# Kernel tuning notes

Measured on AMD Instinct MI355X. Metric: run time of the kernel, lower is better.

## Reference

```python
import jax, jax.numpy as jnp
import numpy as np

B, T, C, H = 512, 256, 512, 64  # batch, block_size, n_embedding, head_size


def setup_inputs() -> dict:
    key = jax.random.key(0)
    kx, kq, kk, kv = jax.random.split(key, 4)
    # nn.Linear(C, H, bias=False) default init ~ U(-1/sqrt(C), 1/sqrt(C)); stored as x @ W
    s = 1.0 / np.sqrt(C)
    return {
        "x": jax.random.normal(kx, (B, T, C), dtype=jnp.float32),
        "Wq": jax.random.uniform(kq, (C, H), jnp.float32, -s, s),
        "Wk": jax.random.uniform(kk, (C, H), jnp.float32, -s, s),
        "Wv": jax.random.uniform(kv, (C, H), jnp.float32, -s, s),
    }


def reference(x, Wq, Wk, Wv):
    # Projections (bias=False Linear)
    q = x @ Wq  # [B,T,H]
    k = x @ Wk  # [B,T,H]
    v = x @ Wv  # [B,T,H]
    scale = k.shape[-1] ** -0.5
    wei = jnp.einsum('bqh,bkh->bqk', q, k) * scale  # [B,T,T]
    causal = jnp.tril(jnp.ones((x.shape[1], x.shape[1]), dtype=bool))
    wei = jnp.where(causal, wei, -jnp.inf)
    wei = jax.nn.softmax(wei, axis=-1)
    # dropout p=0.0 (eval-mode reference) -> identity
    return wei @ v  # [B,T,H]
```

## Files before the change

kernel.cpp:

```cpp
#include <hip/hip_runtime.h>
#include <hip/hip_bf16.h>

typedef __bf16 bf16;
typedef __bf16 bf16x8 __attribute__((ext_vector_type(8)));
typedef __bf16 bf16x4 __attribute__((ext_vector_type(4)));
typedef float  f32x4  __attribute__((ext_vector_type(4)));

#define MFMA16(a,b,c) __builtin_amdgcn_mfma_f32_16x16x32_bf16((a),(b),(c),0,0,0)

__device__ __forceinline__ void gld16(const void* g, void* l) {
    __builtin_amdgcn_global_load_lds(
        (const __attribute__((address_space(1))) void*)g,
        (__attribute__((address_space(3))) void*)l, 16, 0, 0);
}


__global__ void __launch_bounds__(256) wt_frag_kernel(
        const float* __restrict__ Wq, const float* __restrict__ Wk,
        const float* __restrict__ Wv, bf16* __restrict__ WTfrag) {
    int tid = blockIdx.x * 256 + threadIdx.x;
    int j  = tid & 7;
    int l  = (tid >> 3) & 63;
    int f  = tid >> 9;
    int nf = f % 12;
    int KC = f / 12;
    int k   = KC * 32 + (l >> 4) * 8 + j;
    int col = (nf & 3) * 16 + (l & 15);
    const float* W = (nf < 4) ? Wq : ((nf < 8) ? Wk : Wv);
    WTfrag[tid] = (bf16)W[k * 64 + col];
}

__global__ void __launch_bounds__(256, 2) fused_kernel(
        const float* __restrict__ x, const bf16* __restrict__ WTfrag,
        float* __restrict__ out) {
    extern __shared__ char smem[];

    const int tid = threadIdx.x;
    const int l   = tid & 63;
    const int w   = tid >> 6;
    const int lo  = l & 15;
    const int hi  = l >> 4;
    const int b   = blockIdx.x;
    const char* xb = (const char*)x + (size_t)b * 524288;
    const char* wb = (const char*)WTfrag;

    f32x4 acc[4][12];
    #pragma unroll
    for (int mq = 0; mq < 4; ++mq)
        #pragma unroll
        for (int nf = 0; nf < 12; ++nf)
            acc[mq][nf] = (f32x4){0.f, 0.f, 0.f, 0.f};

    #pragma unroll 1
    for (int kc = 0; kc < 16; ++kc) {
        #pragma unroll
        for (int j = 0; j < 8; ++j) {
            const int s   = j * 256 + tid;
            const int row = s >> 3;
            const int uP  = s & 7;
            const int uL  = uP ^ (row & 7);
            gld16(xb + (size_t)row * 2048 + kc * 128 + uL * 16,
                  smem + s * 16);
        }
        #pragma unroll
        for (int j = 0; j < 3; ++j) {
            const int s = j * 256 + tid;
            gld16(wb + kc * 12288 + s * 16, smem + 32768 + s * 16);
        }
        __syncthreads();

        bf16x8 a[4];
        #pragma unroll
        for (int mq = 0; mq < 4; ++mq) {
            const int row = mq * 64 + w * 16 + lo;
            const int u0  = (hi * 2)     ^ (lo & 7);
            const int u1  = (hi * 2 + 1) ^ (lo & 7);
            f32x4 v0 = *(const f32x4*)(smem + row * 128 + u0 * 16);
            f32x4 v1 = *(const f32x4*)(smem + row * 128 + u1 * 16);
            bf16x8 t;
            t[0] = (bf16)v0[0]; t[1] = (bf16)v0[1]; t[2] = (bf16)v0[2]; t[3] = (bf16)v0[3];
            t[4] = (bf16)v1[0]; t[5] = (bf16)v1[1]; t[6] = (bf16)v1[2]; t[7] = (bf16)v1[3];
            a[mq] = t;
        }
        #pragma unroll
        for (int nf = 0; nf < 12; ++nf) {
            bf16x8 bf_ = *(const bf16x8*)(smem + 32768 + nf * 1024 + l * 16);
            #pragma unroll
            for (int mq = 0; mq < 4; ++mq)
                acc[mq][nf] = MFMA16(a[mq], bf_, acc[mq][nf]);
        }
        __syncthreads();
    }

    char* Kb = smem;
    char* Vb = smem + 32768;
    #pragma unroll
    for (int nf = 4; nf < 12; ++nf) {
        #pragma unroll
        for (int mq = 0; mq < 4; ++mq) {
            if (nf < 8) {
                #pragma unroll
                for (int i = 0; i < 4; ++i) {
                    bf16 v = (bf16)acc[mq][nf][i];
                    const int row = mq * 64 + w * 16 + hi * 4 + i;
                    const int col = (nf - 4) * 16 + lo;
                    const int u   = col >> 3;
                    *(bf16*)(Kb + row * 128 + ((u ^ (row & 7)) << 4) +
                             (col & 7) * 2) = v;
                }
            } else {
                const int h  = (nf - 8) * 16 + lo;
                const int tb = mq * 64 + w * 16 + hi * 4;
                const int u  = tb >> 3;
                bf16x4 pk;
                pk[0] = (bf16)acc[mq][nf][0]; pk[1] = (bf16)acc[mq][nf][1];
                pk[2] = (bf16)acc[mq][nf][2]; pk[3] = (bf16)acc[mq][nf][3];
                *(bf16x4*)(Vb + h * 512 + ((u ^ (h & 7)) << 4) +
                           (tb & 7) * 2) = pk;
            }
        }
    }

    bf16* Pl = (bf16*)(smem + 65536) + w * 1152;
    bf16x8 qfr[4][2];
    #pragma unroll
    for (int qf = 0; qf < 4; ++qf) {
        #pragma unroll
        for (int nf = 0; nf < 4; ++nf)
            #pragma unroll
            for (int i = 0; i < 4; ++i)
                Pl[(hi * 4 + i) * 72 + nf * 16 + lo] = (bf16)acc[qf][nf][i];
        #pragma unroll
        for (int ks = 0; ks < 2; ++ks)
            qfr[qf][ks] = *(const bf16x8*)(Pl + lo * 72 + ks * 32 + hi * 8);
    }
    __syncthreads();

    f32x4 o[4][4];
    #pragma unroll
    for (int qf = 0; qf < 4; ++qf)
        #pragma unroll
        for (int mf = 0; mf < 4; ++mf)
            o[qf][mf] = (f32x4){0.f, 0.f, 0.f, 0.f};
    float m2[4]   = {-INFINITY, -INFINITY, -INFINITY, -INFINITY};
    float lsum[4] = {0.f, 0.f, 0.f, 0.f};

    const float SC = 0.125f * 1.44269504088896340736f;

    #pragma unroll
    for (int kc = 0; kc < 4; ++kc) {
        bf16x8 vf[4][2];
        #pragma unroll
        for (int mf = 0; mf < 4; ++mf)
            #pragma unroll
            for (int ks = 0; ks < 2; ++ks) {
                const int h = mf * 16 + lo;
                const int u = kc * 8 + ks * 4 + hi;
                vf[mf][ks] = *(const bf16x8*)(Vb + h * 512 + ((u ^ (lo & 7)) << 4));
            }

        #pragma unroll
        for (int qf = kc; qf < 4; ++qf) {
            f32x4 s[4];
            #pragma unroll
            for (int kf = 0; kf < 4; ++kf) {
                const int key = kc * 64 + kf * 16 + lo;
                bf16x8 k0 = *(const bf16x8*)(Kb + key * 128 + ((hi ^ (lo & 7)) << 4));
                bf16x8 k1 = *(const bf16x8*)(Kb + key * 128 + (((4 + hi) ^ (lo & 7)) << 4));
                f32x4 t = (f32x4){0.f, 0.f, 0.f, 0.f};
                t = MFMA16(k0, qfr[qf][0], t);
                t = MFMA16(k1, qfr[qf][1], t);
                s[kf] = t;
            }
            float mx = -INFINITY;
            #pragma unroll
            for (int kf = 0; kf < 4; ++kf)
                #pragma unroll
                for (int i = 0; i < 4; ++i) {
                    float v = s[kf][i] * SC;
                    if (kc == qf && (kf * 16 + hi * 4 + i) > (w * 16 + lo)) v = -INFINITY;
                    s[kf][i] = v;
                    mx = fmaxf(mx, v);
                }
            mx = fmaxf(mx, __shfl_xor(mx, 16));
            mx = fmaxf(mx, __shfl_xor(mx, 32));
            const float mnew = fmaxf(m2[qf], mx);
            const float rsc  = exp2f(m2[qf] - mnew);
            m2[qf] = mnew;

            float cs = 0.f;
            bf16x4 pk[4];
            #pragma unroll
            for (int kf = 0; kf < 4; ++kf)
                #pragma unroll
                for (int i = 0; i < 4; ++i) {
                    float p = exp2f(s[kf][i] - mnew);
                    cs += p;
                    pk[kf][i] = (bf16)p;
                }
            cs += __shfl_xor(cs, 16);
            cs += __shfl_xor(cs, 32);
            lsum[qf] = lsum[qf] * rsc + cs;

            #pragma unroll
            for (int kf = 0; kf < 4; ++kf)
                *(bf16x4*)(Pl + lo * 72 + kf * 16 + hi * 4) = pk[kf];

            #pragma unroll
            for (int mf = 0; mf < 4; ++mf) {
                o[qf][mf][0] *= rsc; o[qf][mf][1] *= rsc;
                o[qf][mf][2] *= rsc; o[qf][mf][3] *= rsc;
            }
            #pragma unroll
            for (int ks = 0; ks < 2; ++ks) {
                bf16x8 pf = *(const bf16x8*)(Pl + lo * 72 + ks * 32 + hi * 8);
                #pragma unroll
                for (int mf = 0; mf < 4; ++mf)
                    o[qf][mf] = MFMA16(vf[mf][ks], pf, o[qf][mf]);
            }
        }
    }

    #pragma unroll
    for (int qf = 0; qf < 4; ++qf) {
        const float inv = 1.0f / lsum[qf];
        const int q = qf * 64 + w * 16 + lo;
        #pragma unroll
        for (int mf = 0; mf < 4; ++mf) {
            f32x4 r4;
            r4[0] = o[qf][mf][0] * inv; r4[1] = o[qf][mf][1] * inv;
            r4[2] = o[qf][mf][2] * inv; r4[3] = o[qf][mf][3] * inv;
            *(f32x4*)(out + (b * 256 + q) * 64 + mf * 16 + hi * 4) = r4;
        }
    }
}

extern "C" void kernel_launch(void* const* d_in, const int* in_sizes, int n_in,
                              void* d_out, int out_size, void* d_ws, size_t ws_size,
                              hipStream_t stream) {
    const float* x  = (const float*)d_in[0];
    const float* Wq = (const float*)d_in[1];
    const float* Wk = (const float*)d_in[2];
    const float* Wv = (const float*)d_in[3];
    float* out = (float*)d_out;

    bf16* WTfrag = (bf16*)d_ws;

    wt_frag_kernel<<<dim3(384), dim3(256), 0, stream>>>(Wq, Wk, Wv, WTfrag);
    fused_kernel<<<dim3(512), dim3(256), 74752, stream>>>(x, WTfrag, out);
}
```

Baseline: 71.45 us.

## Double-buffer projection loads and use 8 waves with balanced causal row pairing

Moves to 512 threads (8 waves) per block. Each wave owns two 16-row query fragments paired as w and 15-w so causal attention work is balanced across waves. The projection loop now double-buffers the x and weight tiles in LDS, so loads for the next K chunk are issued while the current chunk's MFMAs run. In exchange it uses more LDS (90KB), allows only one block per CU, and halves per-wave accumulator count.

```diff
diff --git a/kernel.cpp b/kernel.cpp
--- a/kernel.cpp
+++ b/kernel.cpp
@@ -30,7 +30,7 @@
     WTfrag[tid] = (bf16)W[k * 64 + col];
 }
 
-__global__ void __launch_bounds__(256, 2) fused_kernel(
+__global__ void __launch_bounds__(512, 1) fused_kernel(
         const float* __restrict__ x, const bf16* __restrict__ WTfrag,
         float* __restrict__ out) {
     extern __shared__ char smem[];
@@ -41,42 +41,52 @@
     const int lo  = l & 15;
     const int hi  = l >> 4;
     const int b   = blockIdx.x;
+    const int fr0 = w;
+    const int fr1 = 15 - w;
     const char* xb = (const char*)x + (size_t)b * 524288;
     const char* wb = (const char*)WTfrag;
 
-    f32x4 acc[4][12];
-    #pragma unroll
-    for (int mq = 0; mq < 4; ++mq)
+    f32x4 acc[2][12];
+    #pragma unroll
+    for (int mq = 0; mq < 2; ++mq)
         #pragma unroll
         for (int nf = 0; nf < 12; ++nf)
             acc[mq][nf] = (f32x4){0.f, 0.f, 0.f, 0.f};
 
+    auto stage = [&](int kc) {
+        const int p = kc & 1;
+        #pragma unroll
+        for (int j = 0; j < 4; ++j) {
+            const int s   = j * 512 + tid;
+            const int row = s >> 3;
+            const int uL  = (s & 7) ^ (row & 7);
+            gld16(xb + (size_t)row * 2048 + kc * 128 + uL * 16,
+                  smem + p * 32768 + s * 16);
+        }
+        gld16(wb + kc * 12288 + tid * 16,
+              smem + 65536 + p * 12288 + tid * 16);
+        if (tid < 256)
+            gld16(wb + kc * 12288 + (512 + tid) * 16,
+                  smem + 65536 + p * 12288 + (512 + tid) * 16);
+    };
+
+    stage(0);
+    __syncthreads();
+
     #pragma unroll 1
     for (int kc = 0; kc < 16; ++kc) {
-        #pragma unroll
-        for (int j = 0; j < 8; ++j) {
-            const int s   = j * 256 + tid;
-            const int row = s >> 3;
-            const int uP  = s & 7;
-            const int uL  = uP ^ (row & 7);
-            gld16(xb + (size_t)row * 2048 + kc * 128 + uL * 16,
-                  smem + s * 16);
-        }
-        #pragma unroll
-        for (int j = 0; j < 3; ++j) {
-            const int s = j * 256 + tid;
-            gld16(wb + kc * 12288 + s * 16, smem + 32768 + s * 16);
-        }
-        __syncthreads();
-
-        bf16x8 a[4];
-        #pragma unroll
-        for (int mq = 0; mq < 4; ++mq) {
-            const int row = mq * 64 + w * 16 + lo;
+        if (kc < 15) stage(kc + 1);
+        const char* xlds  = smem + (kc & 1) * 32768;
+        const char* wtlds = smem + 65536 + (kc & 1) * 12288;
+        bf16x8 a[2];
+        #pragma unroll
+        for (int mq = 0; mq < 2; ++mq) {
+            const int fr  = mq ? fr1 : fr0;
+            const int row = fr * 16 + lo;
             const int u0  = (hi * 2)     ^ (lo & 7);
             const int u1  = (hi * 2 + 1) ^ (lo & 7);
-            f32x4 v0 = *(const f32x4*)(smem + row * 128 + u0 * 16);
-            f32x4 v1 = *(const f32x4*)(smem + row * 128 + u1 * 16);
+            f32x4 v0 = *(const f32x4*)(xlds + row * 128 + u0 * 16);
+            f32x4 v1 = *(const f32x4*)(xlds + row * 128 + u1 * 16);
             bf16x8 t;
             t[0] = (bf16)v0[0]; t[1] = (bf16)v0[1]; t[2] = (bf16)v0[2]; t[3] = (bf16)v0[3];
             t[4] = (bf16)v1[0]; t[5] = (bf16)v1[1]; t[6] = (bf16)v1[2]; t[7] = (bf16)v1[3];
@@ -84,10 +94,9 @@
         }
         #pragma unroll
         for (int nf = 0; nf < 12; ++nf) {
-            bf16x8 bf_ = *(const bf16x8*)(smem + 32768 + nf * 1024 + l * 16);
-            #pragma unroll
-            for (int mq = 0; mq < 4; ++mq)
-                acc[mq][nf] = MFMA16(a[mq], bf_, acc[mq][nf]);
+            bf16x8 bf_ = *(const bf16x8*)(wtlds + nf * 1024 + l * 16);
+            acc[0][nf] = MFMA16(a[0], bf_, acc[0][nf]);
+            acc[1][nf] = MFMA16(a[1], bf_, acc[1][nf]);
         }
         __syncthreads();
     }
@@ -95,60 +104,61 @@
     char* Kb = smem;
     char* Vb = smem + 32768;
     #pragma unroll
-    for (int nf = 4; nf < 12; ++nf) {
-        #pragma unroll
-        for (int mq = 0; mq < 4; ++mq) {
-            if (nf < 8) {
-                #pragma unroll
-                for (int i = 0; i < 4; ++i) {
-                    bf16 v = (bf16)acc[mq][nf][i];
-                    const int row = mq * 64 + w * 16 + hi * 4 + i;
-                    const int col = (nf - 4) * 16 + lo;
-                    const int u   = col >> 3;
-                    *(bf16*)(Kb + row * 128 + ((u ^ (row & 7)) << 4) +
-                             (col & 7) * 2) = v;
-                }
-            } else {
-                const int h  = (nf - 8) * 16 + lo;
-                const int tb = mq * 64 + w * 16 + hi * 4;
-                const int u  = tb >> 3;
-                bf16x4 pk;
-                pk[0] = (bf16)acc[mq][nf][0]; pk[1] = (bf16)acc[mq][nf][1];
-                pk[2] = (bf16)acc[mq][nf][2]; pk[3] = (bf16)acc[mq][nf][3];
-                *(bf16x4*)(Vb + h * 512 + ((u ^ (h & 7)) << 4) +
-                           (tb & 7) * 2) = pk;
-            }
+    for (int mq = 0; mq < 2; ++mq) {
+        const int fr = mq ? fr1 : fr0;
+        #pragma unroll
+        for (int nf = 4; nf < 8; ++nf) {
+            #pragma unroll
+            for (int i = 0; i < 4; ++i) {
+                bf16 v = (bf16)acc[mq][nf][i];
+                const int row = fr * 16 + hi * 4 + i;
+                const int col = (nf - 4) * 16 + lo;
+                const int u   = col >> 3;
+                *(bf16*)(Kb + row * 128 + ((u ^ (row & 7)) << 4) +
+                         (col & 7) * 2) = v;
+            }
+        }
+        #pragma unroll
+        for (int nf = 8; nf < 12; ++nf) {
+            const int h  = (nf - 8) * 16 + lo;
+            const int tb = fr * 16 + hi * 4;
+            const int u  = tb >> 3;
+            bf16x4 pk;
+            pk[0] = (bf16)acc[mq][nf][0]; pk[1] = (bf16)acc[mq][nf][1];
+            pk[2] = (bf16)acc[mq][nf][2]; pk[3] = (bf16)acc[mq][nf][3];
+            *(bf16x4*)(Vb + h * 512 + ((u ^ (h & 7)) << 4) + (tb & 7) * 2) = pk;
         }
     }
 
     bf16* Pl = (bf16*)(smem + 65536) + w * 1152;
-    bf16x8 qfr[4][2];
-    #pragma unroll
-    for (int qf = 0; qf < 4; ++qf) {
+    bf16x8 qfr[2][2];
+    #pragma unroll
+    for (int qi = 0; qi < 2; ++qi) {
         #pragma unroll
         for (int nf = 0; nf < 4; ++nf)
             #pragma unroll
             for (int i = 0; i < 4; ++i)
-                Pl[(hi * 4 + i) * 72 + nf * 16 + lo] = (bf16)acc[qf][nf][i];
+                Pl[(hi * 4 + i) * 72 + nf * 16 + lo] = (bf16)acc[qi][nf][i];
         #pragma unroll
         for (int ks = 0; ks < 2; ++ks)
-            qfr[qf][ks] = *(const bf16x8*)(Pl + lo * 72 + ks * 32 + hi * 8);
+            qfr[qi][ks] = *(const bf16x8*)(Pl + lo * 72 + ks * 32 + hi * 8);
     }
     __syncthreads();
 
-    f32x4 o[4][4];
-    #pragma unroll
-    for (int qf = 0; qf < 4; ++qf)
+    f32x4 o[2][4];
+    #pragma unroll
+    for (int qi = 0; qi < 2; ++qi)
         #pragma unroll
         for (int mf = 0; mf < 4; ++mf)
-            o[qf][mf] = (f32x4){0.f, 0.f, 0.f, 0.f};
-    float m2[4]   = {-INFINITY, -INFINITY, -INFINITY, -INFINITY};
-    float lsum[4] = {0.f, 0.f, 0.f, 0.f};
+            o[qi][mf] = (f32x4){0.f, 0.f, 0.f, 0.f};
+    float m2[2]   = {-INFINITY, -INFINITY};
+    float lsum[2] = {0.f, 0.f};
 
     const float SC = 0.125f * 1.44269504088896340736f;
 
     #pragma unroll
     for (int kc = 0; kc < 4; ++kc) {
+        if (kc > (fr1 >> 2)) continue;
         bf16x8 vf[4][2];
         #pragma unroll
         for (int mf = 0; mf < 4; ++mf)
@@ -160,7 +170,9 @@
             }
 
         #pragma unroll
-        for (int qf = kc; qf < 4; ++qf) {
+        for (int qi = 0; qi < 2; ++qi) {
+            const int f = qi ? fr1 : fr0;
+            if (kc > (f >> 2)) continue;
             f32x4 s[4];
             #pragma unroll
             for (int kf = 0; kf < 4; ++kf) {
@@ -168,25 +180,27 @@
                 bf16x8 k0 = *(const bf16x8*)(Kb + key * 128 + ((hi ^ (lo & 7)) << 4));
                 bf16x8 k1 = *(const bf16x8*)(Kb + key * 128 + (((4 + hi) ^ (lo & 7)) << 4));
                 f32x4 t = (f32x4){0.f, 0.f, 0.f, 0.f};
-                t = MFMA16(k0, qfr[qf][0], t);
-                t = MFMA16(k1, qfr[qf][1], t);
+                t = MFMA16(k0, qfr[qi][0], t);
+                t = MFMA16(k1, qfr[qi][1], t);
                 s[kf] = t;
             }
             float mx = -INFINITY;
+            const bool diag = (kc == (f >> 2));
+            const int qpos  = (f & 3) * 16 + lo;
             #pragma unroll
             for (int kf = 0; kf < 4; ++kf)
                 #pragma unroll
                 for (int i = 0; i < 4; ++i) {
                     float v = s[kf][i] * SC;
-                    if (kc == qf && (kf * 16 + hi * 4 + i) > (w * 16 + lo)) v = -INFINITY;
+                    if (diag && (kf * 16 + hi * 4 + i) > qpos) v = -INFINITY;
                     s[kf][i] = v;
                     mx = fmaxf(mx, v);
                 }
             mx = fmaxf(mx, __shfl_xor(mx, 16));
             mx = fmaxf(mx, __shfl_xor(mx, 32));
-            const float mnew = fmaxf(m2[qf], mx);
-            const float rsc  = exp2f(m2[qf] - mnew);
-            m2[qf] = mnew;
+            const float mnew = fmaxf(m2[qi], mx);
+            const float rsc  = exp2f(m2[qi] - mnew);
+            m2[qi] = mnew;
 
             float cs = 0.f;
             bf16x4 pk[4];
@@ -200,7 +214,7 @@
                 }
             cs += __shfl_xor(cs, 16);
             cs += __shfl_xor(cs, 32);
-            lsum[qf] = lsum[qf] * rsc + cs;
+            lsum[qi] = lsum[qi] * rsc + cs;
 
             #pragma unroll
             for (int kf = 0; kf < 4; ++kf)
@@ -208,28 +222,29 @@
 
             #pragma unroll
             for (int mf = 0; mf < 4; ++mf) {
-                o[qf][mf][0] *= rsc; o[qf][mf][1] *= rsc;
-                o[qf][mf][2] *= rsc; o[qf][mf][3] *= rsc;
+                o[qi][mf][0] *= rsc; o[qi][mf][1] *= rsc;
+                o[qi][mf][2] *= rsc; o[qi][mf][3] *= rsc;
             }
             #pragma unroll
             for (int ks = 0; ks < 2; ++ks) {
                 bf16x8 pf = *(const bf16x8*)(Pl + lo * 72 + ks * 32 + hi * 8);
                 #pragma unroll
                 for (int mf = 0; mf < 4; ++mf)
-                    o[qf][mf] = MFMA16(vf[mf][ks], pf, o[qf][mf]);
-            }
-        }
-    }
-
-    #pragma unroll
-    for (int qf = 0; qf < 4; ++qf) {
-        const float inv = 1.0f / lsum[qf];
-        const int q = qf * 64 + w * 16 + lo;
+                    o[qi][mf] = MFMA16(vf[mf][ks], pf, o[qi][mf]);
+            }
+        }
+    }
+
+    #pragma unroll
+    for (int qi = 0; qi < 2; ++qi) {
+        const int f = qi ? fr1 : fr0;
+        const float inv = 1.0f / lsum[qi];
+        const int q = f * 16 + lo;
         #pragma unroll
         for (int mf = 0; mf < 4; ++mf) {
             f32x4 r4;
-            r4[0] = o[qf][mf][0] * inv; r4[1] = o[qf][mf][1] * inv;
-            r4[2] = o[qf][mf][2] * inv; r4[3] = o[qf][mf][3] * inv;
+            r4[0] = o[qi][mf][0] * inv; r4[1] = o[qi][mf][1] * inv;
+            r4[2] = o[qi][mf][2] * inv; r4[3] = o[qi][mf][3] * inv;
             *(f32x4*)(out + (b * 256 + q) * 64 + mf * 16 + hi * 4) = r4;
         }
     }
@@ -247,5 +262,5 @@
     bf16* WTfrag = (bf16*)d_ws;
 
     wt_frag_kernel<<<dim3(384), dim3(256), 0, stream>>>(Wq, Wk, Wv, WTfrag);
-    fused_kernel<<<dim3(512), dim3(256), 74752, stream>>>(x, WTfrag, out);
-}
+    fused_kernel<<<dim3(512), dim3(512), 90112, stream>>>(x, WTfrag, out);
+}
```

Measured after the change: 81.02 us. 1.13x slower.
